# Optimization experiments

Measured on AMD Instinct MI355X. Metric: run time of the kernel, lower is better.

Reference implementation:

```python
import jax, jax.numpy as jnp
import numpy as np

NP, P, NS = 5, 5, 15  # body parts, joints per part, segments per scale


def _gauss_forward(x):
    # x: (batch, nb_frames, joints=NP*P, coordinates, 1)
    b, T, J, C, _ = x.shape
    inp = x.reshape(b, T, NP, P, C, 1)
    # lengths of the 6 temporal windows: full, two halves, three thirds
    seg_lens = [T, T // 2, T - T // 2, T // 3, T // 3, T - 2 * (T // 3)]
    outs = []
    for L in seg_lens:
        nb_fr = L // NS
        # first NS-1 segments of nb_fr frames each, always starting at frame 0
        head = inp[:, :(NS - 1) * nb_fr].reshape(b, NS - 1, nb_fr, NP, P, C, 1)
        mu_h = head.mean(axis=2)                    # (b, NS-1, NP, P, C, 1)
        xc = head - mu_h[:, :, None]
        cov_h = jnp.einsum('bkfnpci,bkfnpdi->bknpcd', xc, xc) / nb_fr
        # last segment runs to the END of the full sequence (faithful to original)
        tail = inp[:, (NS - 1) * nb_fr:]
        rest = tail.shape[1]
        mu_t = tail.mean(axis=1)                    # (b, NP, P, C, 1)
        xt = tail - mu_t[:, None]
        cov_t = jnp.einsum('bfnpci,bfnpdi->bnpcd', xt, xt) / rest
        mu = jnp.concatenate([mu_h, mu_t[:, None]], axis=1)    # (b, NS, NP, P, C, 1)
        cov = jnp.concatenate([cov_h, cov_t[:, None]], axis=1)  # (b, NS, NP, P, C, C)
        # match torch layout (b, NP, NS, P, ...)
        mu = jnp.transpose(mu, (0, 2, 1, 3, 4, 5))
        cov = jnp.transpose(cov, (0, 2, 1, 3, 4, 5))
        muT = jnp.swapaxes(mu, -1, -2)
        elt00 = cov + mu @ muT                       # E[xx^T]
        ones = jnp.ones(mu.shape[:-2] + (1, 1), dtype=x.dtype)
        top = jnp.concatenate([elt00, mu], axis=-1)
        bot = jnp.concatenate([muT, ones], axis=-1)
        outs.append(jnp.concatenate([top, bot], axis=-2))
    # (b, 6, NP, NS, P, C+1, C+1)
    return jnp.stack(outs, axis=1)


def setup_inputs() -> dict:
    key = jax.random.key(0)
    x = jax.random.normal(key, (256, 2048, 25, 3, 1), dtype=jnp.float32)
    return {"x": x}


def reference(x):
    return _gauss_forward(x)
```

## Files before the change

kernel.cpp:

```cpp
#include <hip/hip_runtime.h>
#include <hip/hip_bf16.h>


__global__ __launch_bounds__(256) void gauss_kernel(const float* __restrict__ x,
                                                    float* __restrict__ out) {
    __shared__ float lds[2250];
    __shared__ float red[225];
    __shared__ float outm[400];

    int bid   = blockIdx.x;
    int chunk = bid % 15;
    int tmp   = bid / 15;
    int stype = tmp % 3;
    int b     = tmp / 3;

    const int nbs[3] = {136, 68, 45};
    int ns = nbs[stype];
    int f0 = chunk * ns;
    int f1 = (chunk == 14) ? 2048 : (f0 + ns);
    float inv_n = 1.0f / (float)(f1 - f0);

    int tid = threadIdx.x;
    if (tid < 250) {
        int j    = tid % 25;
        int tsub = tid / 25;
        const float* base = x + (size_t)b * (2048 * 75) + j * 3;
        float s0=0.f,s1=0.f,s2=0.f,s3=0.f,s4=0.f,s5=0.f,s6=0.f,s7=0.f,s8=0.f;
        for (int t = f0 + tsub; t < f1; t += 10) {
            const float* p = base + t * 75;
            float x0 = p[0], x1 = p[1], x2 = p[2];
            s0 += x0;     s1 += x1;     s2 += x2;
            s3 += x0*x0;  s4 += x0*x1;  s5 += x0*x2;
            s6 += x1*x1;  s7 += x1*x2;  s8 += x2*x2;
        }
        float* l = &lds[tid * 9];
        l[0]=s0; l[1]=s1; l[2]=s2; l[3]=s3; l[4]=s4; l[5]=s5; l[6]=s6; l[7]=s7; l[8]=s8;
    }
    __syncthreads();

    if (tid < 225) {
        int j = tid / 9, si = tid % 9;
        float v = 0.f;
        #pragma unroll
        for (int ts = 0; ts < 10; ++ts) v += lds[(ts * 25 + j) * 9 + si];
        red[j * 9 + si] = v;
    }
    __syncthreads();

    if (tid < 25) {
        const float* r = &red[tid * 9];
        float mu0 = r[0]*inv_n, mu1 = r[1]*inv_n, mu2 = r[2]*inv_n;
        float m00 = r[3]*inv_n, m01 = r[4]*inv_n, m02 = r[5]*inv_n;
        float m11 = r[6]*inv_n, m12 = r[7]*inv_n, m22 = r[8]*inv_n;
        float* o = &outm[tid * 16];
        o[0]=m00; o[1]=m01; o[2]=m02; o[3]=mu0;
        o[4]=m01; o[5]=m11; o[6]=m12; o[7]=mu1;
        o[8]=m02; o[9]=m12; o[10]=m22; o[11]=mu2;
        o[12]=mu0; o[13]=mu1; o[14]=mu2; o[15]=1.0f;
    }
    __syncthreads();

    int so0  = (stype == 0) ? 0 : (stype == 1) ? 1 : 3;
    int ndup = (stype == 0) ? 1 : (stype == 1) ? 2 : 3;
    int total = 400 * ndup;
    size_t obase = (size_t)b * 36000 + (size_t)chunk * 80;
    for (int idx = tid; idx < total; idx += 256) {
        int dup = idx / 400;
        int r   = idx % 400;
        int np  = r / 80;
        int rem = r % 80;
        out[obase + (size_t)(so0 + dup) * 6000 + (size_t)np * 1200 + rem] = outm[r];
    }
}

extern "C" void kernel_launch(void* const* d_in, const int* in_sizes, int n_in,
                              void* d_out, int out_size, void* d_ws, size_t ws_size,
                              hipStream_t stream) {
    const float* x = (const float*)d_in[0];
    float* out = (float*)d_out;
    int blocks = 256 * 3 * 15;
    gauss_kernel<<<blocks, 256, 0, stream>>>(x, out);
}
```

Baseline: 277.9 us.

## Split frames into shared boundary pieces and reduce partial moments in a second pass

```diff
diff --git a/kernel.cpp b/kernel.cpp
--- a/kernel.cpp
+++ b/kernel.cpp
@@ -1,10 +1,50 @@
 #include <hip/hip_runtime.h>
 #include <hip/hip_bf16.h>
-
-
-__global__ __launch_bounds__(256) void gauss_kernel(const float* __restrict__ x,
-                                                    float* __restrict__ out) {
+#include <stdint.h>
+
+
+#define MAXP 64
+struct PieceTab { int n; uint32_t p[MAXP]; };
+
+__global__ __launch_bounds__(256) void p1_kernel(const float* __restrict__ x,
+                                                 float* __restrict__ ws,
+                                                 PieceTab tab) {
     __shared__ float lds[2250];
+    int pc = blockIdx.x;
+    int b  = blockIdx.y;
+    uint32_t pk = tab.p[pc];
+    int f0  = pk & 0xffff;
+    int len = pk >> 16;
+
+    int tid = threadIdx.x;
+    if (tid < 250) {
+        int j = tid % 25, tsub = tid / 25;
+        const float* base = x + (size_t)b * 153600 + (size_t)f0 * 75 + j * 3;
+        float s0=0.f,s1=0.f,s2=0.f,s3=0.f,s4=0.f,s5=0.f,s6=0.f,s7=0.f,s8=0.f;
+        #pragma unroll 5
+        for (int t = tsub; t < len; t += 10) {
+            const float* p = base + (size_t)t * 75;
+            float x0 = p[0], x1 = p[1], x2 = p[2];
+            s0 += x0;     s1 += x1;     s2 += x2;
+            s3 += x0*x0;  s4 += x0*x1;  s5 += x0*x2;
+            s6 += x1*x1;  s7 += x1*x2;  s8 += x2*x2;
+        }
+        float* l = &lds[tid * 9];
+        l[0]=s0; l[1]=s1; l[2]=s2; l[3]=s3; l[4]=s4; l[5]=s5; l[6]=s6; l[7]=s7; l[8]=s8;
+    }
+    __syncthreads();
+
+    if (tid < 225) {
+        float v = 0.f;
+        #pragma unroll
+        for (int ts = 0; ts < 10; ++ts) v += lds[ts * 225 + tid];
+        ws[((size_t)b * tab.n + pc) * 225 + tid] = v;
+    }
+}
+
+__global__ __launch_bounds__(256) void p2_kernel(const float* __restrict__ ws,
+                                                 float* __restrict__ out,
+                                                 PieceTab tab) {
     __shared__ float red[225];
     __shared__ float outm[400];
 
@@ -16,34 +56,19 @@
 
     const int nbs[3] = {136, 68, 45};
     int ns = nbs[stype];
-    int f0 = chunk * ns;
-    int f1 = (chunk == 14) ? 2048 : (f0 + ns);
-    float inv_n = 1.0f / (float)(f1 - f0);
+    int nfr = (chunk == 14) ? (2048 - 14 * ns) : ns;
+    float inv_n = 1.0f / (float)nfr;
 
     int tid = threadIdx.x;
-    if (tid < 250) {
-        int j    = tid % 25;
-        int tsub = tid / 25;
-        const float* base = x + (size_t)b * (2048 * 75) + j * 3;
-        float s0=0.f,s1=0.f,s2=0.f,s3=0.f,s4=0.f,s5=0.f,s6=0.f,s7=0.f,s8=0.f;
-        for (int t = f0 + tsub; t < f1; t += 10) {
-            const float* p = base + t * 75;
-            float x0 = p[0], x1 = p[1], x2 = p[2];
-            s0 += x0;     s1 += x1;     s2 += x2;
-            s3 += x0*x0;  s4 += x0*x1;  s5 += x0*x2;
-            s6 += x1*x1;  s7 += x1*x2;  s8 += x2*x2;
-        }
-        float* l = &lds[tid * 9];
-        l[0]=s0; l[1]=s1; l[2]=s2; l[3]=s3; l[4]=s4; l[5]=s5; l[6]=s6; l[7]=s7; l[8]=s8;
-    }
-    __syncthreads();
-
     if (tid < 225) {
-        int j = tid / 9, si = tid % 9;
         float v = 0.f;
-        #pragma unroll
-        for (int ts = 0; ts < 10; ++ts) v += lds[(ts * 25 + j) * 9 + si];
-        red[j * 9 + si] = v;
+        const float* wb = ws + (size_t)b * tab.n * 225 + tid;
+        for (int p = 0; p < tab.n; ++p) {
+            int f0 = tab.p[p] & 0xffff;
+            int c = f0 / ns; if (c > 14) c = 14;
+            if (c == chunk) v += wb[(size_t)p * 225];
+        }
+        red[tid] = v;
     }
     __syncthreads();
 
@@ -73,11 +98,111 @@
     }
 }
 
+__global__ __launch_bounds__(256) void gauss_fallback(const float* __restrict__ x,
+                                                      float* __restrict__ out) {
+    __shared__ float lds[2250];
+    __shared__ float red[225];
+    __shared__ float outm[400];
+
+    int bid   = blockIdx.x;
+    int chunk = bid % 15;
+    int tmp   = bid / 15;
+    int stype = tmp % 3;
+    int b     = tmp / 3;
+
+    const int nbs[3] = {136, 68, 45};
+    int ns = nbs[stype];
+    int f0 = chunk * ns;
+    int f1 = (chunk == 14) ? 2048 : (f0 + ns);
+    float inv_n = 1.0f / (float)(f1 - f0);
+
+    int tid = threadIdx.x;
+    if (tid < 250) {
+        int j    = tid % 25;
+        int tsub = tid / 25;
+        const float* base = x + (size_t)b * 153600 + j * 3;
+        float s0=0.f,s1=0.f,s2=0.f,s3=0.f,s4=0.f,s5=0.f,s6=0.f,s7=0.f,s8=0.f;
+        for (int t = f0 + tsub; t < f1; t += 10) {
+            const float* p = base + (size_t)t * 75;
+            float x0 = p[0], x1 = p[1], x2 = p[2];
+            s0 += x0;     s1 += x1;     s2 += x2;
+            s3 += x0*x0;  s4 += x0*x1;  s5 += x0*x2;
+            s6 += x1*x1;  s7 += x1*x2;  s8 += x2*x2;
+        }
+        float* l = &lds[tid * 9];
+        l[0]=s0; l[1]=s1; l[2]=s2; l[3]=s3; l[4]=s4; l[5]=s5; l[6]=s6; l[7]=s7; l[8]=s8;
+    }
+    __syncthreads();
+    if (tid < 225) {
+        float v = 0.f;
+        #pragma unroll
+        for (int ts = 0; ts < 10; ++ts) v += lds[ts * 225 + tid];
+        red[tid] = v;
+    }
+    __syncthreads();
+    if (tid < 25) {
+        const float* r = &red[tid * 9];
+        float mu0 = r[0]*inv_n, mu1 = r[1]*inv_n, mu2 = r[2]*inv_n;
+        float m00 = r[3]*inv_n, m01 = r[4]*inv_n, m02 = r[5]*inv_n;
+        float m11 = r[6]*inv_n, m12 = r[7]*inv_n, m22 = r[8]*inv_n;
+        float* o = &outm[tid * 16];
+        o[0]=m00; o[1]=m01; o[2]=m02; o[3]=mu0;
+        o[4]=m01; o[5]=m11; o[6]=m12; o[7]=mu1;
+        o[8]=m02; o[9]=m12; o[10]=m22; o[11]=mu2;
+        o[12]=mu0; o[13]=mu1; o[14]=mu2; o[15]=1.0f;
+    }
+    __syncthreads();
+    int so0  = (stype == 0) ? 0 : (stype == 1) ? 1 : 3;
+    int ndup = (stype == 0) ? 1 : (stype == 1) ? 2 : 3;
+    int total = 400 * ndup;
+    size_t obase = (size_t)b * 36000 + (size_t)chunk * 80;
+    for (int idx = tid; idx < total; idx += 256) {
+        int dup = idx / 400;
+        int r   = idx % 400;
+        int np  = r / 80;
+        int rem = r % 80;
+        out[obase + (size_t)(so0 + dup) * 6000 + (size_t)np * 1200 + rem] = outm[r];
+    }
+}
+
+static int build_pieces(uint32_t* pk) {
+    unsigned char isb[2049];
+    for (int i = 0; i <= 2048; ++i) isb[i] = 0;
+    isb[2048] = 1;
+    for (int k = 1; k <= 14; ++k) { isb[45*k] = 1; isb[68*k] = 1; isb[136*k] = 1; }
+    int n = 0, prev = 0;
+    for (int f = 1; f <= 2048; ++f) {
+        if (!isb[f]) continue;
+        int len = f - prev;
+        int np = (len + 49) / 50;
+        int base = len / np, rem = len % np;
+        int s = prev;
+        for (int i = 0; i < np; ++i) {
+            int l = base + (i < rem ? 1 : 0);
+            pk[n++] = (uint32_t)(s | (l << 16));
+            s += l;
+        }
+        prev = f;
+    }
+    return n;
+}
+
 extern "C" void kernel_launch(void* const* d_in, const int* in_sizes, int n_in,
                               void* d_out, int out_size, void* d_ws, size_t ws_size,
                               hipStream_t stream) {
     const float* x = (const float*)d_in[0];
     float* out = (float*)d_out;
-    int blocks = 256 * 3 * 15;
-    gauss_kernel<<<blocks, 256, 0, stream>>>(x, out);
-}
+
+    PieceTab tab;
+    tab.n = build_pieces(tab.p);
+    size_t need = (size_t)256 * tab.n * 225 * sizeof(float);
+
+    if (ws_size >= need && tab.n <= MAXP) {
+        float* ws = (float*)d_ws;
+        dim3 g1(tab.n, 256);
+        p1_kernel<<<g1, 256, 0, stream>>>(x, ws, tab);
+        p2_kernel<<<256 * 45, 256, 0, stream>>>(ws, out, tab);
+    } else {
+        gauss_fallback<<<256 * 45, 256, 0, stream>>>(x, out);
+    }
+}
```

New measurement: 333.1 us. +19.8%, slower.

## Split into partial-sum pieces at segment boundaries then combine per segment

Applied to the files above, without the earlier changes.

```diff
diff --git a/kernel.cpp b/kernel.cpp
--- a/kernel.cpp
+++ b/kernel.cpp
@@ -1,57 +1,162 @@
 #include <hip/hip_runtime.h>
 #include <hip/hip_bf16.h>
-
-
-__global__ __launch_bounds__(256) void gauss_kernel(const float* __restrict__ x,
-                                                    float* __restrict__ out) {
+#include <stdint.h>
+
+
+#define NPIECE_MAX 64
+struct Tab {
+    int n;
+    uint32_t p[NPIECE_MAX];
+    uint32_t cr[45];
+};
+
+__global__ __launch_bounds__(256) void p1_kernel(const float* __restrict__ x,
+                                                 float* __restrict__ ws, Tab tab) {
+    __shared__ float sx[3756];
+    int pc = blockIdx.x, b = blockIdx.y;
+    uint32_t pk = tab.p[pc];
+    int f0 = pk & 0xffff, L = (int)(pk >> 16);
+    int w0 = f0 * 75;
+    int base_f = w0 & ~3;
+    int shift = w0 - base_f;
+    int nv4 = (shift + L * 75 + 3) >> 2;
+    const float4* src = (const float4*)(x + (size_t)b * 153600 + base_f);
+    int tid = threadIdx.x;
+    for (int i = tid; i < nv4; i += 256)
+        ((float4*)sx)[i] = src[i];
+    __syncthreads();
+
+    float s[9] = {0,0,0,0,0,0,0,0,0};
+    if (tid < 250) {
+        int j = tid % 25, ts = tid / 25;
+        for (int t = ts; t < L; t += 10) {
+            const float* p = &sx[shift + t * 75 + j * 3];
+            float a = p[0], bb = p[1], c = p[2];
+            s[0]+=a;    s[1]+=bb;   s[2]+=c;
+            s[3]+=a*a;  s[4]+=a*bb; s[5]+=a*c;
+            s[6]+=bb*bb; s[7]+=bb*c; s[8]+=c*c;
+        }
+    }
+    __syncthreads();
+    if (tid < 250) {
+        float* l = &sx[tid * 9];
+        #pragma unroll
+        for (int k = 0; k < 9; ++k) l[k] = s[k];
+    }
+    __syncthreads();
+    if (tid < 225) {
+        float v = 0.f;
+        #pragma unroll
+        for (int ts = 0; ts < 10; ++ts) v += sx[ts * 225 + tid];
+        ws[((size_t)b * tab.n + pc) * 225 + tid] = v;
+    }
+}
+
+__global__ __launch_bounds__(256) void p2_kernel(const float* __restrict__ ws,
+                                                 float* __restrict__ out, Tab tab) {
+    __shared__ float sws[2520];
+    __shared__ float red[2025];
+    __shared__ float invn[45];
+    int b = blockIdx.x, np = blockIdx.y;
+    int tid = threadIdx.x;
+    int n = tab.n;
+    int tot = n * 45;
+    const float* wb = ws + (size_t)b * n * 225 + np * 45;
+    for (int i = tid; i < tot; i += 256) {
+        int piece = i / 45, idx = i - piece * 45;
+        sws[i] = wb[(size_t)piece * 225 + idx];
+    }
+    if (tid < 45) {
+        int st = tid / 15, ch = tid - st * 15;
+        const int nst[3] = {136, 68, 45};
+        int ns = nst[st];
+        int nfr = (ch == 14) ? (2048 - 14 * ns) : ns;
+        invn[tid] = 1.0f / (float)nfr;
+    }
+    __syncthreads();
+
+    for (int i = tid; i < 2025; i += 256) {
+        int sc = i / 45, idx = i - sc * 45;
+        uint32_t r = tab.cr[sc];
+        int p0 = (int)(r & 0xffff), p1 = (int)(r >> 16);
+        float v = 0.f;
+        for (int p = p0; p < p1; ++p) v += sws[p * 45 + idx];
+        red[i] = v;
+    }
+    __syncthreads();
+
+    float* ob = out + (size_t)b * 36000 + (size_t)np * 1200;
+    for (int o = tid; o < 7200; o += 256) {
+        int seg = o / 1200;
+        int r1  = o - seg * 1200;
+        int ch  = r1 / 80;
+        int r3  = r1 - ch * 80;
+        int p   = r3 >> 4;
+        int e   = r3 & 15;
+        int st  = (seg == 0) ? 0 : (seg < 3) ? 1 : 2;
+        int sc  = st * 15 + ch;
+        int r   = e >> 2, c = e & 3;
+        float v;
+        if (r == 3 && c == 3) {
+            v = 1.0f;
+        } else {
+            int mi;
+            if (r == 3) mi = c;
+            else if (c == 3) mi = r;
+            else {
+                int lo = (r < c) ? r : c;
+                int hi = r + c - lo;
+                mi = 3 + ((lo * (5 - lo)) >> 1) + hi;
+            }
+            v = red[sc * 45 + p * 9 + mi] * invn[sc];
+        }
+        ob[(size_t)seg * 6000 + r1] = v;
+    }
+}
+
+__global__ __launch_bounds__(256) void gauss_fallback(const float* __restrict__ x,
+                                                      float* __restrict__ out) {
     __shared__ float lds[2250];
     __shared__ float red[225];
     __shared__ float outm[400];
-
-    int bid   = blockIdx.x;
+    int bid = blockIdx.x;
     int chunk = bid % 15;
-    int tmp   = bid / 15;
+    int tmp = bid / 15;
     int stype = tmp % 3;
-    int b     = tmp / 3;
-
+    int b = tmp / 3;
     const int nbs[3] = {136, 68, 45};
     int ns = nbs[stype];
     int f0 = chunk * ns;
     int f1 = (chunk == 14) ? 2048 : (f0 + ns);
     float inv_n = 1.0f / (float)(f1 - f0);
-
     int tid = threadIdx.x;
     if (tid < 250) {
-        int j    = tid % 25;
-        int tsub = tid / 25;
-        const float* base = x + (size_t)b * (2048 * 75) + j * 3;
+        int j = tid % 25, tsub = tid / 25;
+        const float* base = x + (size_t)b * 153600 + j * 3;
         float s0=0.f,s1=0.f,s2=0.f,s3=0.f,s4=0.f,s5=0.f,s6=0.f,s7=0.f,s8=0.f;
         for (int t = f0 + tsub; t < f1; t += 10) {
-            const float* p = base + t * 75;
+            const float* p = base + (size_t)t * 75;
             float x0 = p[0], x1 = p[1], x2 = p[2];
-            s0 += x0;     s1 += x1;     s2 += x2;
-            s3 += x0*x0;  s4 += x0*x1;  s5 += x0*x2;
-            s6 += x1*x1;  s7 += x1*x2;  s8 += x2*x2;
+            s0+=x0; s1+=x1; s2+=x2;
+            s3+=x0*x0; s4+=x0*x1; s5+=x0*x2;
+            s6+=x1*x1; s7+=x1*x2; s8+=x2*x2;
         }
         float* l = &lds[tid * 9];
         l[0]=s0; l[1]=s1; l[2]=s2; l[3]=s3; l[4]=s4; l[5]=s5; l[6]=s6; l[7]=s7; l[8]=s8;
     }
     __syncthreads();
-
     if (tid < 225) {
-        int j = tid / 9, si = tid % 9;
         float v = 0.f;
         #pragma unroll
-        for (int ts = 0; ts < 10; ++ts) v += lds[(ts * 25 + j) * 9 + si];
-        red[j * 9 + si] = v;
-    }
-    __syncthreads();
-
+        for (int ts = 0; ts < 10; ++ts) v += lds[ts * 225 + tid];
+        red[tid] = v;
+    }
+    __syncthreads();
     if (tid < 25) {
         const float* r = &red[tid * 9];
-        float mu0 = r[0]*inv_n, mu1 = r[1]*inv_n, mu2 = r[2]*inv_n;
-        float m00 = r[3]*inv_n, m01 = r[4]*inv_n, m02 = r[5]*inv_n;
-        float m11 = r[6]*inv_n, m12 = r[7]*inv_n, m22 = r[8]*inv_n;
+        float mu0=r[0]*inv_n, mu1=r[1]*inv_n, mu2=r[2]*inv_n;
+        float m00=r[3]*inv_n, m01=r[4]*inv_n, m02=r[5]*inv_n;
+        float m11=r[6]*inv_n, m12=r[7]*inv_n, m22=r[8]*inv_n;
         float* o = &outm[tid * 16];
         o[0]=m00; o[1]=m01; o[2]=m02; o[3]=mu0;
         o[4]=m01; o[5]=m11; o[6]=m12; o[7]=mu1;
@@ -59,17 +164,50 @@
         o[12]=mu0; o[13]=mu1; o[14]=mu2; o[15]=1.0f;
     }
     __syncthreads();
-
-    int so0  = (stype == 0) ? 0 : (stype == 1) ? 1 : 3;
+    int so0 = (stype == 0) ? 0 : (stype == 1) ? 1 : 3;
     int ndup = (stype == 0) ? 1 : (stype == 1) ? 2 : 3;
     int total = 400 * ndup;
     size_t obase = (size_t)b * 36000 + (size_t)chunk * 80;
     for (int idx = tid; idx < total; idx += 256) {
         int dup = idx / 400;
-        int r   = idx % 400;
-        int np  = r / 80;
+        int r = idx % 400;
+        int np = r / 80;
         int rem = r % 80;
         out[obase + (size_t)(so0 + dup) * 6000 + (size_t)np * 1200 + rem] = outm[r];
+    }
+}
+
+static void build_tab(Tab& tab) {
+    unsigned char isb[2049];
+    for (int i = 0; i <= 2048; ++i) isb[i] = 0;
+    isb[2048] = 1;
+    for (int k = 1; k <= 14; ++k) { isb[45*k] = 1; isb[68*k] = 1; isb[136*k] = 1; }
+    int n = 0, prev = 0;
+    int pf0[NPIECE_MAX];
+    for (int f = 1; f <= 2048; ++f) {
+        if (!isb[f]) continue;
+        int len = f - prev;
+        int npc = (len + 49) / 50;
+        int base = len / npc, rem = len % npc;
+        int s = prev;
+        for (int i = 0; i < npc && n < NPIECE_MAX; ++i) {
+            int l = base + (i < rem ? 1 : 0);
+            pf0[n] = s;
+            tab.p[n++] = (uint32_t)(s | (l << 16));
+            s += l;
+        }
+        prev = f;
+    }
+    tab.n = n;
+    const int nst[3] = {136, 68, 45};
+    for (int st = 0; st < 3; ++st) {
+        int ns = nst[st];
+        for (int c = 0; c < 15; ++c) {
+            int a = c * ns, bnd = (c == 14) ? 2048 : (c + 1) * ns;
+            int p0 = 0; while (p0 < n && pf0[p0] < a) ++p0;
+            int p1 = p0; while (p1 < n && pf0[p1] < bnd) ++p1;
+            tab.cr[st * 15 + c] = (uint32_t)(p0 | (p1 << 16));
+        }
     }
 }
 
@@ -78,6 +216,18 @@
                               hipStream_t stream) {
     const float* x = (const float*)d_in[0];
     float* out = (float*)d_out;
-    int blocks = 256 * 3 * 15;
-    gauss_kernel<<<blocks, 256, 0, stream>>>(x, out);
-}
+
+    Tab tab;
+    build_tab(tab);
+    size_t need = (size_t)256 * tab.n * 225 * sizeof(float);
+
+    if (ws_size >= need) {
+        float* ws = (float*)d_ws;
+        dim3 g1(tab.n, 256);
+        p1_kernel<<<g1, 256, 0, stream>>>(x, ws, tab);
+        dim3 g2(256, 5);
+        p2_kernel<<<g2, 256, 0, stream>>>(ws, out, tab);
+    } else {
+        gauss_fallback<<<256 * 45, 256, 0, stream>>>(x, out);
+    }
+}
```

New measurement: 245.3 us. -11.7%, faster.
